# Performance work log

Hardware: AMD Instinct MI355X
Metric: run time of the kernel (lower is better)

## Reference

```python
import jax, jax.numpy as jnp
import numpy as np

N_NODES = 100000
N_EDGES = 1600000
IN_CH, HID_CH, OUT_CH = 128, 128, 64


def glorot(key, fan_in, fan_out):
    lim = np.sqrt(6.0 / (fan_in + fan_out)).astype(np.float32)
    return jax.random.uniform(key, (fan_in, fan_out), jnp.float32, -lim, lim)


def gcn_conv(x, src, dst, W, b):
    """PyG GCNConv: add self-loops, symmetric deg^-1/2 normalization,
    linear transform, scatter-add aggregation at targets, plus bias."""
    n = x.shape[0]
    xw = x @ W  # [N, F_out]
    loop = jnp.arange(n)
    s = jnp.concatenate([src, loop])  # sources (message origin)
    d = jnp.concatenate([dst, loop])  # targets (aggregation site)
    deg = jax.ops.segment_sum(jnp.ones_like(d, dtype=xw.dtype), d, num_segments=n)
    dinv = jnp.where(deg > 0, jax.lax.rsqrt(deg), 0.0)
    norm = dinv[s] * dinv[d]  # [E+N]
    out = jax.ops.segment_sum(norm[:, None] * xw[s], d, num_segments=n)
    return out + b


def setup_inputs() -> dict:
    key = jax.random.key(0)
    ks = jax.random.split(key, 8)
    x = jax.random.normal(ks[0], (N_NODES, IN_CH), jnp.float32)
    edge_index = jax.random.randint(ks[1], (2, N_EDGES), 0, N_NODES, jnp.int64)
    return {
        "x": x,
        "edge_index": edge_index,
        "W1": glorot(ks[2], IN_CH, HID_CH),
        "b1": jnp.zeros((HID_CH,), jnp.float32),
        "W2": glorot(ks[3], HID_CH, HID_CH),
        "b2": jnp.zeros((HID_CH,), jnp.float32),
        "W3": glorot(ks[4], HID_CH, OUT_CH),
        "b3": jnp.zeros((OUT_CH,), jnp.float32),
    }


def reference(x, edge_index, W1, b1, W2, b2, W3, b3):
    src, dst = edge_index[0], edge_index[1]
    # eval mode: dropout is identity
    h = jax.nn.relu(gcn_conv(x, src, dst, W1, b1))
    h = jax.nn.relu(gcn_conv(h, src, dst, W2, b2))
    h = gcn_conv(h, src, dst, W3, b3)
    return jax.nn.log_softmax(h, axis=1)
```

## Files before the change

### kernel.cpp

```cpp
#include <hip/hip_runtime.h>
#include <math.h>


#define NN 100000
#define NE 1600000
#define NBUK 391
#define BCAP 4608

typedef float floatx4 __attribute__((ext_vector_type(4)));
typedef short short8 __attribute__((ext_vector_type(8)));

__device__ __forceinline__ unsigned short f2bf(float f) {
    unsigned u = __float_as_uint(f);
    unsigned r = (u + 0x7fffu + ((u >> 16) & 1u)) >> 16;
    return (unsigned short)r;
}
__device__ __forceinline__ float bflo(unsigned u) { return __uint_as_float(u << 16); }
__device__ __forceinline__ float bfhi(unsigned u) { return __uint_as_float(u & 0xffff0000u); }

__global__ __launch_bounds__(256) void k_wprep(const float* __restrict__ W, unsigned short* __restrict__ Wtg,
                                               int K, int NC) {
    int idx = blockIdx.x * 256 + threadIdx.x;
    if (idx >= NC * K) return;
    int n = idx / K, k = idx - n * K;
    Wtg[idx] = f2bf(W[k * NC + n]);
}

__global__ __launch_bounds__(256) void k_bucket(const int4* __restrict__ src4, const int4* __restrict__ dst4,
                                                int* __restrict__ bcur, int* __restrict__ bbuf, int E) {
    __shared__ int hist[NBUK];
    __shared__ int base[NBUK];
    int t = threadIdx.x;
    for (int b = t; b < NBUK; b += 256) hist[b] = 0;
    __syncthreads();
    int E4 = E >> 2;
    int q0 = blockIdx.x * 1024;
    #pragma unroll
    for (int j = 0; j < 4; j++) {
        int q = q0 + j * 256 + t;
        if (q < E4) {
            int4 d = dst4[q];
            atomicAdd(&hist[d.x >> 8], 1);
            atomicAdd(&hist[d.y >> 8], 1);
            atomicAdd(&hist[d.z >> 8], 1);
            atomicAdd(&hist[d.w >> 8], 1);
        }
    }
    __syncthreads();
    for (int b = t; b < NBUK; b += 256) {
        int c = hist[b];
        base[b] = c ? atomicAdd(&bcur[b], c) : 0;
        hist[b] = 0;
    }
    __syncthreads();
    #pragma unroll
    for (int j = 0; j < 4; j++) {
        int q = q0 + j * 256 + t;
        if (q < E4) {
            int4 s = src4[q];
            int4 d = dst4[q];
            int sv[4] = {s.x, s.y, s.z, s.w};
            int dv[4] = {d.x, d.y, d.z, d.w};
            #pragma unroll
            for (int u = 0; u < 4; u++) {
                int b = dv[u] >> 8;
                int r = atomicAdd(&hist[b], 1);
                int pos = base[b] + r;
                if (pos < BCAP) bbuf[b * BCAP + pos] = (sv[u] << 8) | (dv[u] & 255);
            }
        }
    }
}

__global__ void k_scanbuckets(const int* __restrict__ bcur, int* __restrict__ bbase, int nb,
                              int* __restrict__ row_ptr, int n, int E) {
    int lane = threadIdx.x;
    int carry = 0;
    for (int base = 0; base < nb; base += 64) {
        int idx = base + lane;
        int v = (idx < nb) ? min(bcur[idx], BCAP) : 0;
        int orig = v;
        #pragma unroll
        for (int o = 1; o < 64; o <<= 1) {
            int u = __shfl_up(v, o);
            if (lane >= o) v += u;
        }
        if (idx < nb) bbase[idx] = carry + v - orig;
        carry += __shfl(v, 63);
    }
    if (lane == 0) row_ptr[n] = E;
}

__global__ __launch_bounds__(256) void k_build(const int* __restrict__ bcur, const int* __restrict__ bbase,
                                               const int* __restrict__ bbuf,
                                               int* __restrict__ row_ptr, int* __restrict__ csr, int N) {
    __shared__ int sh[256];
    __shared__ int cur[256];
    __shared__ int loc[BCAP];
    int b = blockIdx.x, t = threadIdx.x;
    int cnt = min(bcur[b], BCAP);
    int gbase = bbase[b];
    const int* bp = bbuf + b * BCAP;
    sh[t] = 0;
    __syncthreads();
    for (int i = t; i < cnt; i += 256) atomicAdd(&sh[bp[i] & 255], 1);
    __syncthreads();
    int v = sh[t];
    for (int o = 1; o < 256; o <<= 1) {
        int u = (t >= o) ? sh[t - o] : 0;
        __syncthreads();
        sh[t] += u;
        __syncthreads();
    }
    int excl = sh[t] - v;
    int node = b * 256 + t;
    if (node < N) row_ptr[node] = gbase + excl;
    cur[t] = excl;
    __syncthreads();
    for (int i = t; i < cnt; i += 256) {
        int p = bp[i];
        int r = atomicAdd(&cur[p & 255], 1);
        loc[r] = p >> 8;
    }
    __syncthreads();
    {
        int seg0 = excl;
        int seg1 = cur[t];
        for (int i = seg0 + 1; i < seg1; i++) {
            int val = loc[i];
            int j = i - 1;
            while (j >= seg0 && loc[j] > val) {
                loc[j + 1] = loc[j];
                j--;
            }
            loc[j + 1] = val;
        }
    }
    __syncthreads();
    for (int i = t; i < cnt; i += 256) csr[gbase + i] = loc[i];
}

__global__ __launch_bounds__(256) void k_dinv(const int* __restrict__ row_ptr, float* __restrict__ dinv, int n) {
    int i = blockIdx.x * 256 + threadIdx.x;
    if (i < n) {
        int d = row_ptr[i + 1] - row_ptr[i];
        dinv[i] = rsqrtf((float)d + 1.0f);
    }
}


template <int NC, bool CVT>
__global__ __launch_bounds__(256) void k_mfma(const void* __restrict__ Av, const unsigned short* __restrict__ Wtg,
                                              const float* __restrict__ dinv, unsigned short* __restrict__ Y, int M) {
    constexpr int K = 128;
    constexpr int NT = NC / 16;
    __shared__ unsigned short Wt[NC][136];
    int t = threadIdx.x;
    constexpr int NV = NC * K / 8;
    for (int idx = t; idx < NV; idx += 256) {
        int nrow = idx >> 4;
        int chunk = idx & 15;
        *(uint4*)&Wt[nrow][chunk * 8] = *(const uint4*)(Wtg + nrow * K + chunk * 8);
    }
    __syncthreads();
    int lane = t & 63, wid = t >> 6;
    int col = lane & 15, quad = lane >> 4;
    int nstrips = M / 16;
    int s = blockIdx.x * 4 + wid;
    if (s >= nstrips) return;
    int row0 = s * 16;

    short8 af[4];
    if (CVT) {
        const float* Af = (const float*)Av + (size_t)(row0 + col) * K + quad * 8;
        #pragma unroll
        for (int ks = 0; ks < 4; ks++) {
            float4 f0 = *(const float4*)(Af + ks * 32);
            float4 f1 = *(const float4*)(Af + ks * 32 + 4);
            short8 v;
            v[0] = (short)f2bf(f0.x); v[1] = (short)f2bf(f0.y); v[2] = (short)f2bf(f0.z); v[3] = (short)f2bf(f0.w);
            v[4] = (short)f2bf(f1.x); v[5] = (short)f2bf(f1.y); v[6] = (short)f2bf(f1.z); v[7] = (short)f2bf(f1.w);
            af[ks] = v;
        }
    } else {
        const unsigned short* Ab = (const unsigned short*)Av + (size_t)(row0 + col) * K + quad * 8;
        #pragma unroll
        for (int ks = 0; ks < 4; ks++) af[ks] = *(const short8*)(Ab + ks * 32);
    }

    floatx4 acc[NT];
    #pragma unroll
    for (int i = 0; i < NT; i++) acc[i] = (floatx4){0.f, 0.f, 0.f, 0.f};
    #pragma unroll
    for (int ks = 0; ks < 4; ks++) {
        #pragma unroll
        for (int nt = 0; nt < NT; nt++) {
            short8 bfrag = *(const short8*)&Wt[nt * 16 + col][ks * 32 + quad * 8];
            acc[nt] = __builtin_amdgcn_mfma_f32_16x16x32_bf16(af[ks], bfrag, acc[nt], 0, 0, 0);
        }
    }
    #pragma unroll
    for (int r = 0; r < 4; r++) {
        int row = row0 + quad * 4 + r;
        float dv = dinv[row];
        #pragma unroll
        for (int nt = 0; nt < NT; nt++) {
            Y[(size_t)row * NC + nt * 16 + col] = f2bf(acc[nt][r] * dv);
        }
    }
}


__device__ __forceinline__ void acc8(float* a, uint4 v) {
    a[0] += bflo(v.x); a[1] += bfhi(v.x);
    a[2] += bflo(v.y); a[3] += bfhi(v.y);
    a[4] += bflo(v.z); a[5] += bfhi(v.z);
    a[6] += bflo(v.w); a[7] += bfhi(v.w);
}

__global__ __launch_bounds__(256) void k_gather_relu_bf(const uint4* __restrict__ y, const int* __restrict__ csr,
                                                        const int* __restrict__ row_ptr, const float* __restrict__ dinv,
                                                        const float* __restrict__ bias, uint4* __restrict__ h, int n) {
    int node = blockIdx.x * 16 + (threadIdx.x >> 4);
    int c = threadIdx.x & 15;
    if (node >= n) return;
    int s0 = row_ptr[node], s1 = row_ptr[node + 1];
    float a[8] = {};
    acc8(a, y[(size_t)node * 16 + c]);
    int p = s0;
    for (; p + 4 <= s1; p += 4) {
        int i0 = csr[p], i1 = csr[p + 1], i2 = csr[p + 2], i3 = csr[p + 3];
        uint4 v0 = y[(size_t)i0 * 16 + c];
        uint4 v1 = y[(size_t)i1 * 16 + c];
        uint4 v2 = y[(size_t)i2 * 16 + c];
        uint4 v3 = y[(size_t)i3 * 16 + c];
        acc8(a, v0); acc8(a, v1); acc8(a, v2); acc8(a, v3);
    }
    for (; p < s1; p++) acc8(a, y[(size_t)csr[p] * 16 + c]);
    float s = dinv[node];
    float4 b0 = ((const float4*)bias)[c * 2];
    float4 b1 = ((const float4*)bias)[c * 2 + 1];
    float r0 = fmaxf(s * a[0] + b0.x, 0.f), r1 = fmaxf(s * a[1] + b0.y, 0.f);
    float r2 = fmaxf(s * a[2] + b0.z, 0.f), r3 = fmaxf(s * a[3] + b0.w, 0.f);
    float r4 = fmaxf(s * a[4] + b1.x, 0.f), r5 = fmaxf(s * a[5] + b1.y, 0.f);
    float r6 = fmaxf(s * a[6] + b1.z, 0.f), r7 = fmaxf(s * a[7] + b1.w, 0.f);
    uint4 o;
    o.x = ((unsigned)f2bf(r1) << 16) | f2bf(r0);
    o.y = ((unsigned)f2bf(r3) << 16) | f2bf(r2);
    o.z = ((unsigned)f2bf(r5) << 16) | f2bf(r4);
    o.w = ((unsigned)f2bf(r7) << 16) | f2bf(r6);
    h[(size_t)node * 16 + c] = o;
}

__global__ __launch_bounds__(256) void k_gather_lsm_bf(const uint4* __restrict__ y, const int* __restrict__ csr,
                                                       const int* __restrict__ row_ptr, const float* __restrict__ dinv,
                                                       const float* __restrict__ bias, float4* __restrict__ out4, int n) {
    int node = blockIdx.x * 32 + (threadIdx.x >> 3);
    int c = threadIdx.x & 7;
    if (node >= n) return;
    int s0 = row_ptr[node], s1 = row_ptr[node + 1];
    float a[8] = {};
    acc8(a, y[(size_t)node * 8 + c]);
    int p = s0;
    for (; p + 4 <= s1; p += 4) {
        int i0 = csr[p], i1 = csr[p + 1], i2 = csr[p + 2], i3 = csr[p + 3];
        uint4 v0 = y[(size_t)i0 * 8 + c];
        uint4 v1 = y[(size_t)i1 * 8 + c];
        uint4 v2 = y[(size_t)i2 * 8 + c];
        uint4 v3 = y[(size_t)i3 * 8 + c];
        acc8(a, v0); acc8(a, v1); acc8(a, v2); acc8(a, v3);
    }
    for (; p < s1; p++) acc8(a, y[(size_t)csr[p] * 8 + c]);
    float s = dinv[node];
    float4 b0 = ((const float4*)bias)[c * 2];
    float4 b1 = ((const float4*)bias)[c * 2 + 1];
    float v[8];
    v[0] = s * a[0] + b0.x; v[1] = s * a[1] + b0.y; v[2] = s * a[2] + b0.z; v[3] = s * a[3] + b0.w;
    v[4] = s * a[4] + b1.x; v[5] = s * a[5] + b1.y; v[6] = s * a[6] + b1.z; v[7] = s * a[7] + b1.w;
    float m = v[0];
    #pragma unroll
    for (int i = 1; i < 8; i++) m = fmaxf(m, v[i]);
    #pragma unroll
    for (int o = 4; o > 0; o >>= 1) m = fmaxf(m, __shfl_xor(m, o));
    float sum = 0.f;
    #pragma unroll
    for (int i = 0; i < 8; i++) sum += expf(v[i] - m);
    #pragma unroll
    for (int o = 4; o > 0; o >>= 1) sum += __shfl_xor(sum, o);
    float lse = m + logf(sum);
    out4[(size_t)node * 16 + c * 2]     = make_float4(v[0] - lse, v[1] - lse, v[2] - lse, v[3] - lse);
    out4[(size_t)node * 16 + c * 2 + 1] = make_float4(v[4] - lse, v[5] - lse, v[6] - lse, v[7] - lse);
}


extern "C" void kernel_launch(void* const* d_in, const int* in_sizes, int n_in,
                              void* d_out, int out_size, void* d_ws, size_t ws_size,
                              hipStream_t stream) {
    const float* x  = (const float*)d_in[0];
    const int*   ei = (const int*)d_in[1];
    const float* W1 = (const float*)d_in[2];
    const float* b1 = (const float*)d_in[3];
    const float* W2 = (const float*)d_in[4];
    const float* b2 = (const float*)d_in[5];
    const float* W3 = (const float*)d_in[6];
    const float* b3 = (const float*)d_in[7];
    float* out = (float*)d_out;

    const int N = NN, E = NE;
    const int nb = (N + 255) / 256;

    char* ws = (char*)d_ws;
    size_t off = 0;
    auto alloc = [&](size_t bytes) -> void* {
        void* p = ws + off;
        off += bytes;
        off = (off + 255) & ~(size_t)255;
        return p;
    };
    int*            row_ptr = (int*)alloc((size_t)(N + 1) * 4);
    float*          dinvv   = (float*)alloc((size_t)N * 4);
    int*            bcur    = (int*)alloc(512 * 4);
    int*            bbase   = (int*)alloc(512 * 4);
    int*            bbuf    = (int*)alloc((size_t)NBUK * BCAP * 4);
    int*            csr     = (int*)alloc((size_t)E * 4);
    unsigned short* wt1     = (unsigned short*)alloc(128 * 128 * 2);
    unsigned short* wt2     = (unsigned short*)alloc(128 * 128 * 2);
    unsigned short* wt3     = (unsigned short*)alloc(64 * 128 * 2);
    unsigned short* yb      = (unsigned short*)alloc((size_t)N * 128 * 2);
    unsigned short* hb      = (unsigned short*)alloc((size_t)N * 128 * 2);
    (void)ws_size; (void)in_sizes; (void)n_in; (void)out_size;

    const int* srcp = ei;
    const int* dstp = ei + E;

    hipMemsetAsync(bcur, 0, 512 * 4, stream);
    k_wprep<<<64, 256, 0, stream>>>(W1, wt1, 128, 128);
    k_wprep<<<64, 256, 0, stream>>>(W2, wt2, 128, 128);
    k_wprep<<<32, 256, 0, stream>>>(W3, wt3, 128, 64);
    k_bucket<<<(E + 4095) / 4096, 256, 0, stream>>>((const int4*)srcp, (const int4*)dstp, bcur, bbuf, E);
    k_scanbuckets<<<1, 64, 0, stream>>>(bcur, bbase, NBUK, row_ptr, N, E);
    k_build<<<NBUK, 256, 0, stream>>>(bcur, bbase, bbuf, row_ptr, csr, N);
    k_dinv<<<nb, 256, 0, stream>>>(row_ptr, dinvv, N);

    const int nstrips = N / 16;
    const int gmm = (nstrips + 3) / 4;
    k_mfma<128, true><<<gmm, 256, 0, stream>>>(x, wt1, dinvv, yb, N);
    k_gather_relu_bf<<<N / 16, 256, 0, stream>>>((const uint4*)yb, csr, row_ptr, dinvv, b1, (uint4*)hb, N);
    k_mfma<128, false><<<gmm, 256, 0, stream>>>(hb, wt2, dinvv, yb, N);
    k_gather_relu_bf<<<N / 16, 256, 0, stream>>>((const uint4*)yb, csr, row_ptr, dinvv, b2, (uint4*)hb, N);
    k_mfma<64, false><<<gmm, 256, 0, stream>>>(hb, wt3, dinvv, yb, N);
    k_gather_lsm_bf<<<N / 32, 256, 0, stream>>>((const uint4*)yb, csr, row_ptr, dinvv, b3, (float4*)out, N);
}
```

Before: 378.3 us.

## Make MFMA GEMM persistent with prefetch, stage output in LDS, drop CSR sort

The dense transform kernel becomes grid-stride persistent over 512 blocks. Each wave prefetches the next 16-row strip's A fragments while computing the current one, and the weight tile is loaded into LDS once per block instead of once per strip. Outputs are staged through LDS so global stores become coalesced 16-byte writes instead of scattered 2-byte writes. The per-node insertion sort in CSR build is also removed, so neighbor order within a row becomes nondeterministic; this changes the fp summation order but not the result beyond rounding.

```diff
diff --git a/kernel.cpp b/kernel.cpp
--- a/kernel.cpp
+++ b/kernel.cpp
@@ -123,20 +123,6 @@
         loc[r] = p >> 8;
     }
     __syncthreads();
-    {
-        int seg0 = excl;
-        int seg1 = cur[t];
-        for (int i = seg0 + 1; i < seg1; i++) {
-            int val = loc[i];
-            int j = i - 1;
-            while (j >= seg0 && loc[j] > val) {
-                loc[j + 1] = loc[j];
-                j--;
-            }
-            loc[j + 1] = val;
-        }
-    }
-    __syncthreads();
     for (int i = t; i < cnt; i += 256) csr[gbase + i] = loc[i];
 }
 
@@ -154,7 +140,9 @@
                                               const float* __restrict__ dinv, unsigned short* __restrict__ Y, int M) {
     constexpr int K = 128;
     constexpr int NT = NC / 16;
+    constexpr int NU = NC / 32;
     __shared__ unsigned short Wt[NC][136];
+    __shared__ unsigned short Ost[4][16][NC + 8];
     int t = threadIdx.x;
     constexpr int NV = NC * K / 8;
     for (int idx = t; idx < NV; idx += 256) {
@@ -166,47 +154,72 @@
     int lane = t & 63, wid = t >> 6;
     int col = lane & 15, quad = lane >> 4;
     int nstrips = M / 16;
+    int stride = gridDim.x * 4;
     int s = blockIdx.x * 4 + wid;
     if (s >= nstrips) return;
-    int row0 = s * 16;
-
-    short8 af[4];
-    if (CVT) {
-        const float* Af = (const float*)Av + (size_t)(row0 + col) * K + quad * 8;
+
+    auto loadA = [&](int strip, short8 af[4]) {
+        int row0 = strip * 16;
+        if (CVT) {
+            const float* Af = (const float*)Av + (size_t)(row0 + col) * K + quad * 8;
+            #pragma unroll
+            for (int ks = 0; ks < 4; ks++) {
+                float4 f0 = *(const float4*)(Af + ks * 32);
+                float4 f1 = *(const float4*)(Af + ks * 32 + 4);
+                short8 v;
+                v[0] = (short)f2bf(f0.x); v[1] = (short)f2bf(f0.y); v[2] = (short)f2bf(f0.z); v[3] = (short)f2bf(f0.w);
+                v[4] = (short)f2bf(f1.x); v[5] = (short)f2bf(f1.y); v[6] = (short)f2bf(f1.z); v[7] = (short)f2bf(f1.w);
+                af[ks] = v;
+            }
+        } else {
+            const unsigned short* Ab = (const unsigned short*)Av + (size_t)(row0 + col) * K + quad * 8;
+            #pragma unroll
+            for (int ks = 0; ks < 4; ks++) af[ks] = *(const short8*)(Ab + ks * 32);
+        }
+    };
+
+    short8 cur[4];
+    loadA(s, cur);
+    while (true) {
+        int snext = s + stride;
+        bool has = (snext < nstrips);
+        short8 nxt[4];
+        if (has) loadA(snext, nxt);
+
+        floatx4 acc[NT];
+        #pragma unroll
+        for (int i = 0; i < NT; i++) acc[i] = (floatx4){0.f, 0.f, 0.f, 0.f};
         #pragma unroll
         for (int ks = 0; ks < 4; ks++) {
-            float4 f0 = *(const float4*)(Af + ks * 32);
-            float4 f1 = *(const float4*)(Af + ks * 32 + 4);
-            short8 v;
-            v[0] = (short)f2bf(f0.x); v[1] = (short)f2bf(f0.y); v[2] = (short)f2bf(f0.z); v[3] = (short)f2bf(f0.w);
-            v[4] = (short)f2bf(f1.x); v[5] = (short)f2bf(f1.y); v[6] = (short)f2bf(f1.z); v[7] = (short)f2bf(f1.w);
-            af[ks] = v;
-        }
-    } else {
-        const unsigned short* Ab = (const unsigned short*)Av + (size_t)(row0 + col) * K + quad * 8;
-        #pragma unroll
-        for (int ks = 0; ks < 4; ks++) af[ks] = *(const short8*)(Ab + ks * 32);
-    }
-
-    floatx4 acc[NT];
-    #pragma unroll
-    for (int i = 0; i < NT; i++) acc[i] = (floatx4){0.f, 0.f, 0.f, 0.f};
-    #pragma unroll
-    for (int ks = 0; ks < 4; ks++) {
-        #pragma unroll
-        for (int nt = 0; nt < NT; nt++) {
-            short8 bfrag = *(const short8*)&Wt[nt * 16 + col][ks * 32 + quad * 8];
-            acc[nt] = __builtin_amdgcn_mfma_f32_16x16x32_bf16(af[ks], bfrag, acc[nt], 0, 0, 0);
-        }
-    }
-    #pragma unroll
-    for (int r = 0; r < 4; r++) {
-        int row = row0 + quad * 4 + r;
-        float dv = dinv[row];
-        #pragma unroll
-        for (int nt = 0; nt < NT; nt++) {
-            Y[(size_t)row * NC + nt * 16 + col] = f2bf(acc[nt][r] * dv);
-        }
+            #pragma unroll
+            for (int nt = 0; nt < NT; nt++) {
+                short8 bfrag = *(const short8*)&Wt[nt * 16 + col][ks * 32 + quad * 8];
+                acc[nt] = __builtin_amdgcn_mfma_f32_16x16x32_bf16(cur[ks], bfrag, acc[nt], 0, 0, 0);
+            }
+        }
+        int row0 = s * 16;
+        #pragma unroll
+        for (int r = 0; r < 4; r++) {
+            int row = row0 + quad * 4 + r;
+            float dv = dinv[row];
+            #pragma unroll
+            for (int nt = 0; nt < NT; nt++) {
+                Ost[wid][quad * 4 + r][nt * 16 + col] = f2bf(acc[nt][r] * dv);
+            }
+        }
+        #pragma unroll
+        for (int i = 0; i < NU; i++) {
+            int idx = i * 64 + lane;
+            int rr = idx >> 4, cc = idx & 15;
+            int rr2 = (NC == 128) ? (idx >> 4) : (idx >> 3);
+            int cc2 = (NC == 128) ? (idx & 15) : (idx & 7);
+            (void)rr; (void)cc;
+            ((uint4*)&Y[(size_t)(row0 + rr2) * NC])[cc2] = *(uint4*)&Ost[wid][rr2][cc2 * 8];
+        }
+        if (!has) break;
+        s = snext;
+        #pragma unroll
+        for (int ks = 0; ks < 4; ks++) cur[ks] = nxt[ks];
     }
 }
 
@@ -342,12 +355,10 @@
     k_build<<<NBUK, 256, 0, stream>>>(bcur, bbase, bbuf, row_ptr, csr, N);
     k_dinv<<<nb, 256, 0, stream>>>(row_ptr, dinvv, N);
 
-    const int nstrips = N / 16;
-    const int gmm = (nstrips + 3) / 4;
-    k_mfma<128, true><<<gmm, 256, 0, stream>>>(x, wt1, dinvv, yb, N);
+    k_mfma<128, true><<<512, 256, 0, stream>>>(x, wt1, dinvv, yb, N);
     k_gather_relu_bf<<<N / 16, 256, 0, stream>>>((const uint4*)yb, csr, row_ptr, dinvv, b1, (uint4*)hb, N);
-    k_mfma<128, false><<<gmm, 256, 0, stream>>>(hb, wt2, dinvv, yb, N);
+    k_mfma<128, false><<<512, 256, 0, stream>>>(hb, wt2, dinvv, yb, N);
     k_gather_relu_bf<<<N / 16, 256, 0, stream>>>((const uint4*)yb, csr, row_ptr, dinvv, b2, (uint4*)hb, N);
-    k_mfma<64, false><<<gmm, 256, 0, stream>>>(hb, wt3, dinvv, yb, N);
+    k_mfma<64, false><<<512, 256, 0, stream>>>(hb, wt3, dinvv, yb, N);
     k_gather_lsm_bf<<<N / 32, 256, 0, stream>>>((const uint4*)yb, csr, row_ptr, dinvv, b3, (float4*)out, N);
 }
```

Result: faster. 336.1 us (-11.2%).
